# Kernel tuning notes

Measured on AMD Instinct MI355X. Metric: run time of the kernel, lower is better.

The kernel has to match this reference:

```python
import jax, jax.numpy as jnp
import numpy as np

LN_EPS = 1e-5

def _next_fast_len(n):
    # smallest 5-smooth integer >= n (matches scipy.fftpack.next_fast_len)
    while True:
        m = n
        for p in (2, 3, 5):
            while m % p == 0:
                m //= p
        if m == 1:
            return n
        n += 1

def _conv1d_fft(x, w):
    # x: (b, h, N, d), convolved along axis -2 against w: (h, M) along axis -1.
    # Matches the torch reference: multiply by conj(rfft(w)), roll by -1, take last N.
    N = x.shape[-2]
    M = w.shape[-1]
    L = _next_fast_len(N + M - 1)
    fx = jnp.fft.rfft(x, n=L, axis=-2)                    # (b, h, F, d) complex
    fw = jnp.fft.rfft(w, n=L, axis=-1)                    # (h, F) complex
    out = jnp.fft.irfft(fx * jnp.conj(fw)[..., None], L, axis=-2)
    out = jnp.roll(out, -1, axis=-2)
    return out[..., L - N:, :]                            # (b, h, N, d)

def setup_inputs() -> dict:
    key = jax.random.key(0)
    ks = jax.random.split(key, 5)
    b, n, d, h = 4, 4096, 1024, 8
    dh = d // h
    s = 0.02
    return {
        "x": jax.random.normal(ks[0], (b, n, d), jnp.float32),
        "ln_gamma": jnp.ones((d,), jnp.float32),
        "ln_beta": jnp.zeros((d,), jnp.float32),
        "w_in": jax.random.normal(ks[1], (d, d), jnp.float32) * s,
        "b_in": jnp.zeros((d,), jnp.float32),
        "initial_state": jax.random.normal(ks[2], (h, dh), jnp.float32),
        "alpha": jax.random.normal(ks[3], (h,), jnp.float32),
        "w_out": jax.random.normal(ks[4], (d, d), jnp.float32) * s,
        "b_out": jnp.zeros((d,), jnp.float32),
    }

def reference(x, ln_gamma, ln_beta, w_in, b_in, initial_state, alpha, w_out, b_out):
    b, n, d = x.shape
    h, dh = initial_state.shape
    # LayerNorm
    mu = jnp.mean(x, axis=-1, keepdims=True)
    var = jnp.mean((x - mu) ** 2, axis=-1, keepdims=True)
    xn = (x - mu) * jax.lax.rsqrt(var + LN_EPS) * ln_gamma + ln_beta
    # project_in (torch Linear: y = x @ W.T + b)
    xp = xn @ w_in.T + b_in
    # b n (h d) -> b h n d
    xh = xp.reshape(b, n, h, dh).transpose(0, 2, 1, 3)
    # prepend learned initial state, then first difference along n
    init = jnp.broadcast_to(initial_state[None, :, None, :], (b, h, 1, dh))
    xc = jnp.concatenate([init, xh], axis=2)
    xd = xc[:, :, 1:] - xc[:, :, :-1]                     # (b, h, n, dh)
    # EMA weights per head
    a = jax.nn.sigmoid(alpha)[:, None]                    # (h, 1)
    ar = jnp.arange(n)
    w = a * (1.0 - a) ** ar[::-1]                         # (h, n)
    out = _conv1d_fft(xd, w)
    # initial-state contribution
    init_w = (1.0 - a) ** (ar + 1)                        # (h, n)
    out = out + init_w[:, :, None] * initial_state[:, None, :]
    # b h n d -> b n (h d), then project_out
    out = out.transpose(0, 2, 1, 3).reshape(b, n, d)
    return out @ w_out.T + b_out
```

## Files before the change

kernel.cpp:

```cpp
#include <hip/hip_runtime.h>
#include <stdint.h>

typedef float  f32x4 __attribute__((ext_vector_type(4)));
typedef __bf16 bf16x8 __attribute__((ext_vector_type(8)));
typedef short  s16x8 __attribute__((ext_vector_type(8)));
typedef unsigned short u16;

static __device__ __forceinline__ u16 f2bf(float f) {
  unsigned u = __float_as_uint(f);
  u += 0x7fffu + ((u >> 16) & 1u);
  return (u16)(u >> 16);
}
static __device__ __forceinline__ float bf2f(u16 u) {
  return __uint_as_float(((unsigned)u) << 16);
}

static __device__ __forceinline__ void async_copy16(void* lds, const void* g) {
  __builtin_amdgcn_global_load_lds(
      (const __attribute__((address_space(1))) unsigned int*)g,
      (__attribute__((address_space(3))) unsigned int*)lds, 16, 0, 0);
}

__global__ __launch_bounds__(256) void cvt2_k(const float* __restrict__ in0,
                                              const float* __restrict__ in1,
                                              u16* __restrict__ out0,
                                              u16* __restrict__ out1, int n4) {
  int i = blockIdx.x * 256 + threadIdx.x;
  const float* in = (i < n4) ? in0 : in1;
  u16* out = (i < n4) ? out0 : out1;
  int idx = (i < n4) ? i : i - n4;
  float4 v = reinterpret_cast<const float4*>(in)[idx];
  ushort4 o;
  o.x = f2bf(v.x); o.y = f2bf(v.y); o.z = f2bf(v.z); o.w = f2bf(v.w);
  reinterpret_cast<ushort4*>(out)[idx] = o;
}

__global__ __launch_bounds__(256) void ln_k(const float* __restrict__ x,
                                            const float* __restrict__ g,
                                            const float* __restrict__ b,
                                            u16* __restrict__ xn) {
  const int D = 1024;
  const int row = blockIdx.x;
  const int tid = threadIdx.x;
  const float4 v = reinterpret_cast<const float4*>(x + (size_t)row * D)[tid];
  float s  = v.x + v.y + v.z + v.w;
  float s2 = v.x * v.x + v.y * v.y + v.z * v.z + v.w * v.w;
  #pragma unroll
  for (int off = 32; off > 0; off >>= 1) {
    s  += __shfl_down(s, off);
    s2 += __shfl_down(s2, off);
  }
  __shared__ float red[8];
  const int lane = tid & 63, wv = tid >> 6;
  if (lane == 0) { red[wv] = s; red[4 + wv] = s2; }
  __syncthreads();
  s  = red[0] + red[1] + red[2] + red[3];
  s2 = red[4] + red[5] + red[6] + red[7];
  const float mu   = s * (1.0f / D);
  const float var  = s2 * (1.0f / D) - mu * mu;
  const float rstd = rsqrtf(var + 1e-5f);
  const float4 gv = reinterpret_cast<const float4*>(g)[tid];
  const float4 bv = reinterpret_cast<const float4*>(b)[tid];
  ushort4 o;
  o.x = f2bf((v.x - mu) * rstd * gv.x + bv.x);
  o.y = f2bf((v.y - mu) * rstd * gv.y + bv.y);
  o.z = f2bf((v.z - mu) * rstd * gv.z + bv.z);
  o.w = f2bf((v.w - mu) * rstd * gv.w + bv.w);
  reinterpret_cast<ushort4*>(xn + (size_t)row * D)[tid] = o;
}

template<int MODE>
__global__ __launch_bounds__(512, 2) void gemm_bt_k(const u16* __restrict__ A,
                                                    const u16* __restrict__ Bm,
                                                    const float* __restrict__ bias,
                                                    void* __restrict__ Cv,
                                                    const float* __restrict__ alpha,
                                                    float* __restrict__ Lp,
                                                    int M, int N, int K) {
  const int tid  = threadIdx.x;
  const int lane = tid & 63;
  const int wv   = tid >> 6;
  const int wrr  = wv >> 2;
  const int wcc  = wv & 3;
  const int ntN  = N >> 8;
  const int nwg  = (M >> 8) * ntN;
  const int bid  = blockIdx.x;
  const int wgid = (bid & 7) * (nwg >> 3) + (bid >> 3);
  const int mt = wgid / ntN, nt = wgid % ntN;
  const int m0 = mt << 8, n0 = nt << 8;

  __shared__ __align__(16) u16 smem[65536];
  __shared__ float sRed[256];

  const int u   = tid >> 3;
  const int tch = tid & 7;
  const int csw = (tch ^ (u & 7)) << 3;
  const int lofs = u * 64 + (tch << 3);
  const u16* gA = A  + (size_t)(m0 + u) * K + csw;
  const u16* gB = Bm + (size_t)(n0 + u) * K + csw;

  f32x4 acc[8][4];
  #pragma unroll
  for (int i = 0; i < 8; ++i)
    #pragma unroll
    for (int j = 0; j < 4; ++j) acc[i][j] = f32x4{0.f, 0.f, 0.f, 0.f};

  const int fr  = lane & 15;
  const int fkc = lane >> 4;
  const int sx  = fr & 7;
  const int nk  = K >> 6;
  int buf = 0;

  #pragma unroll
  for (int r = 0; r < 4; ++r) {
    async_copy16(&smem[lofs + r * 4096], gA + (size_t)(r * 64) * K);
    async_copy16(&smem[32768 + lofs + r * 4096], gB + (size_t)(r * 64) * K);
  }
  __syncthreads();

  for (int t = 0; t < nk; ++t) {
    if (t + 1 < nk) {
      const size_t ko = (size_t)(t + 1) << 6;
      const int nb = (buf ^ 1) * 16384;
      #pragma unroll
      for (int r = 0; r < 4; ++r) {
        async_copy16(&smem[nb + lofs + r * 4096], gA + ko + (size_t)(r * 64) * K);
        async_copy16(&smem[32768 + nb + lofs + r * 4096], gB + ko + (size_t)(r * 64) * K);
      }
    }
    const u16* bA = smem + buf * 16384;
    const u16* bB = smem + 32768 + buf * 16384;
    #pragma unroll
    for (int s = 0; s < 2; ++s) {
      const int ch = ((((s << 2) + fkc) ^ sx) << 3);
      s16x8 af[8], bfr[4];
      #pragma unroll
      for (int i = 0; i < 8; ++i)
        af[i] = *reinterpret_cast<const s16x8*>(
            &bA[(wrr * 128 + i * 16 + fr) * 64 + ch]);
      #pragma unroll
      for (int j = 0; j < 4; ++j)
        bfr[j] = *reinterpret_cast<const s16x8*>(
            &bB[(wcc * 64 + j * 16 + fr) * 64 + ch]);
      #pragma unroll
      for (int i = 0; i < 8; ++i)
        #pragma unroll
        for (int j = 0; j < 4; ++j)
          acc[i][j] = __builtin_amdgcn_mfma_f32_16x16x32_bf16(
              __builtin_bit_cast(bf16x8, af[i]),
              __builtin_bit_cast(bf16x8, bfr[j]), acc[i][j], 0, 0, 0);
    }
    __syncthreads();
    buf ^= 1;
  }

  float* sC = (float*)smem;
  const int cr = (lane >> 4) << 2;
  const int cc = lane & 15;
  float bv[4];
  #pragma unroll
  for (int nj = 0; nj < 4; ++nj) bv[nj] = bias[n0 + wcc * 64 + nj * 16 + cc];

  #pragma unroll
  for (int p = 0; p < 2; ++p) {
    __syncthreads();
    if (wrr == p) {
      #pragma unroll
      for (int mi = 0; mi < 8; ++mi)
        #pragma unroll
        for (int nj = 0; nj < 4; ++nj)
          #pragma unroll
          for (int rr = 0; rr < 4; ++rr) {
            const int row = mi * 16 + cr + rr;
            const int col = wcc * 64 + nj * 16 + cc;
            sC[row * 256 + (col ^ ((row & 4) << 2))] = acc[mi][nj][rr] + bv[nj];
          }
    }
    __syncthreads();
    #pragma unroll 4
    for (int it = 0; it < 16; ++it) {
      const int row  = it * 8 + (tid >> 6);
      const int col0 = (tid & 63) * 4;
      f32x4 v = *(const f32x4*)&sC[row * 256 + (col0 ^ ((row & 4) << 2))];
      const size_t goff = (size_t)(m0 + p * 128 + row) * N + n0 + col0;
      if (MODE == 1) {
        ushort4 o; o.x = f2bf(v[0]); o.y = f2bf(v[1]); o.z = f2bf(v[2]); o.w = f2bf(v[3]);
        *(ushort4*)&((u16*)Cv)[goff] = o;
      } else {
        *(f32x4*)&((float*)Cv)[goff] = v;
      }
    }
    if (MODE == 1) {
      const int col = tid & 255;
      const int hh = (n0 + col) >> 7;
      const float a  = 1.0f / (1.0f + __expf(-alpha[hh]));
      const float rw = 1.0f - a;
      float r64 = rw;
      #pragma unroll
      for (int s = 0; s < 6; ++s) r64 *= r64;
      const bool lo = (tid < 256);
      const int rbase  = lo ? 1 : 64;
      const int nsteps = lo ? 63 : 64;
      float prev = sC[(rbase - 1) * 256 + (col ^ (((rbase - 1) & 4) << 2))];
      float L = 0.f;
      #pragma unroll 8
      for (int t = rbase; t < rbase + 64; ++t) {
        if (t - rbase >= nsteps) break;
        const float w = sC[t * 256 + (col ^ ((t & 4) << 2))];
        L = rw * L + a * (w - prev);
        prev = w;
      }
      if (!lo) sRed[col] = L;
      __syncthreads();
      if (lo) {
        const float Lt = r64 * L + sRed[col];
        const int bb = m0 >> 12;
        const int q  = ((m0 >> 7) & 31) + p;
        Lp[((size_t)bb * 32 + q) * 1024 + n0 + col] = Lt;
      }
    }
  }
}

__global__ __launch_bounds__(256) void ema_carry_k(const u16* __restrict__ xpb,
                                                   const float* __restrict__ alpha,
                                                   const float* __restrict__ init,
                                                   float* __restrict__ carry) {
  const int Dd = 1024, nCh = 32;
  const int idx = blockIdx.x * 256 + threadIdx.x;
  const int c  = idx & (Dd - 1);
  const int bb = idx >> 10;
  const int h = c >> 7;
  const float a = 1.0f / (1.0f + __expf(-alpha[h]));
  const float r = 1.0f - a;
  float q_ = r, r127 = 1.0f;
  #pragma unroll
  for (int s = 0; s < 7; ++s) { r127 *= q_; q_ *= q_; }
  const float rT = r127 * r;
  float cin = init[c];
  float prevv = cin;
  for (int q = 0; q < nCh; ++q) {
    const size_t rowb = (size_t)bb * 4096 + (size_t)q * 128;
    const float v0 = bf2f(xpb[rowb * Dd + c]);
    const size_t off = ((size_t)bb * nCh + q) * Dd + c;
    const float L = carry[off] + a * r127 * (v0 - prevv);
    carry[off] = cin;
    cin = rT * cin + L;
    prevv = bf2f(xpb[(rowb + 127) * Dd + c]);
  }
}

__global__ __launch_bounds__(256) void ema_apply_k(const u16* __restrict__ xp,
                                                   const float* __restrict__ alpha,
                                                   const float* __restrict__ init,
                                                   const float* __restrict__ carry,
                                                   u16* __restrict__ ob) {
  const int Nn = 4096, Dd = 1024, T = 128, nCh = 32;
  int bid = blockIdx.x;
  const int cg = bid & 1;  bid >>= 1;
  const int q  = bid & 31; bid >>= 5;
  const int bb = bid;
  const int c = cg * 512 + threadIdx.x * 2;
  const int h = c >> 7;
  const float a = 1.0f / (1.0f + __expf(-alpha[h]));
  const float r = 1.0f - a;
  const u16* px = xp + ((size_t)bb * Nn + (size_t)q * T) * Dd + c;
  u16* po = ob + ((size_t)bb * Nn + (size_t)q * T) * Dd + c;
  float2 Oin = *(const float2*)(carry + ((size_t)bb * nCh + q) * Dd + c);
  float O0 = Oin.x, O1 = Oin.y;
  float p0, p1;
  if (q == 0) { p0 = init[c]; p1 = init[c + 1]; }
  else { ushort2 pv = *(const ushort2*)(px - Dd); p0 = bf2f(pv.x); p1 = bf2f(pv.y); }
  #pragma unroll 4
  for (int t = 0; t < T; ++t) {
    ushort2 v = *(const ushort2*)(px + (size_t)t * Dd);
    float v0 = bf2f(v.x), v1 = bf2f(v.y);
    O0 = r * O0 + a * (v0 - p0);
    O1 = r * O1 + a * (v1 - p1);
    p0 = v0; p1 = v1;
    ushort2 o; o.x = f2bf(O0); o.y = f2bf(O1);
    *(ushort2*)(po + (size_t)t * Dd) = o;
  }
}

extern "C" void kernel_launch(void* const* d_in, const int* in_sizes, int n_in,
                              void* d_out, int out_size, void* d_ws, size_t ws_size,
                              hipStream_t stream) {
  const float* x     = (const float*)d_in[0];
  const float* ln_g  = (const float*)d_in[1];
  const float* ln_b  = (const float*)d_in[2];
  const float* w_in  = (const float*)d_in[3];
  const float* b_in  = (const float*)d_in[4];
  const float* init  = (const float*)d_in[5];
  const float* alpha = (const float*)d_in[6];
  const float* w_out = (const float*)d_in[7];
  const float* b_out = (const float*)d_in[8];
  float* out = (float*)d_out;

  const int B = 4, N = 4096, D = 1024;
  const int M = B * N;

  char* p = (char*)d_ws;
  u16*   xn  = (u16*)p; p += (size_t)M * D * sizeof(u16);
  u16*   wi  = (u16*)p; p += (size_t)D * D * sizeof(u16);
  u16*   wo  = (u16*)p; p += (size_t)D * D * sizeof(u16);
  u16*   xpb = (u16*)p; p += (size_t)M * D * sizeof(u16);
  float* cr  = (float*)p; p += (size_t)B * 32 * D * sizeof(float);
  u16*   ob  = (u16*)p;

  const int n4 = D * D / 4;
  cvt2_k<<<dim3(2 * n4 / 256), dim3(256), 0, stream>>>(w_in, w_out, wi, wo, n4);
  ln_k<<<dim3(M), dim3(256), 0, stream>>>(x, ln_g, ln_b, xn);
  gemm_bt_k<1><<<dim3((M / 256) * (D / 256)), dim3(512), 0, stream>>>(
      xn, wi, b_in, xpb, alpha, cr, M, D, D);
  ema_carry_k<<<dim3(B * D / 256), dim3(256), 0, stream>>>(xpb, alpha, init, cr);
  ema_apply_k<<<dim3(B * 32 * 2), dim3(256), 0, stream>>>(xpb, alpha, init, cr, ob);
  gemm_bt_k<0><<<dim3((M / 256) * (D / 256)), dim3(512), 0, stream>>>(
      ob, wo, b_out, out, nullptr, nullptr, M, D, D);
}
```

Measured before the change: 138.8 us.

## Fuse weight conversion into LayerNorm, prefetch carry loads, widen EMA apply grid

Three changes. First, the weight bf16 conversion kernel is merged into the LayerNorm kernel as extra blocks, which saves one launch. Second, ema_carry_k now loads all 32 chunk values into registers before running the serial recurrence, so the global loads are not stalled behind the dependency chain. Third, ema_apply_k now gives each thread one channel instead of two and launches twice as many blocks, for more parallelism at the cost of narrower 2-byte memory accesses.

```diff
diff --git a/kernel.cpp b/kernel.cpp
--- a/kernel.cpp
+++ b/kernel.cpp
@@ -21,27 +21,28 @@
       (__attribute__((address_space(3))) unsigned int*)lds, 16, 0, 0);
 }
 
-__global__ __launch_bounds__(256) void cvt2_k(const float* __restrict__ in0,
-                                              const float* __restrict__ in1,
-                                              u16* __restrict__ out0,
-                                              u16* __restrict__ out1, int n4) {
-  int i = blockIdx.x * 256 + threadIdx.x;
-  const float* in = (i < n4) ? in0 : in1;
-  u16* out = (i < n4) ? out0 : out1;
-  int idx = (i < n4) ? i : i - n4;
-  float4 v = reinterpret_cast<const float4*>(in)[idx];
-  ushort4 o;
-  o.x = f2bf(v.x); o.y = f2bf(v.y); o.z = f2bf(v.z); o.w = f2bf(v.w);
-  reinterpret_cast<ushort4*>(out)[idx] = o;
-}
-
-__global__ __launch_bounds__(256) void ln_k(const float* __restrict__ x,
-                                            const float* __restrict__ g,
-                                            const float* __restrict__ b,
-                                            u16* __restrict__ xn) {
-  const int D = 1024;
+__global__ __launch_bounds__(256) void ln_cvt_k(const float* __restrict__ x,
+                                                const float* __restrict__ g,
+                                                const float* __restrict__ b,
+                                                u16* __restrict__ xn,
+                                                const float* __restrict__ w0,
+                                                const float* __restrict__ w1,
+                                                u16* __restrict__ o0,
+                                                u16* __restrict__ o1) {
+  const int D = 1024, Mrows = 16384, n4 = 262144;
+  const int tid = threadIdx.x;
+  if (blockIdx.x >= Mrows) {
+    int i = (blockIdx.x - Mrows) * 256 + tid;
+    const float* in = (i < n4) ? w0 : w1;
+    u16* out = (i < n4) ? o0 : o1;
+    int idx = (i < n4) ? i : i - n4;
+    float4 v = reinterpret_cast<const float4*>(in)[idx];
+    ushort4 o;
+    o.x = f2bf(v.x); o.y = f2bf(v.y); o.z = f2bf(v.z); o.w = f2bf(v.w);
+    reinterpret_cast<ushort4*>(out)[idx] = o;
+    return;
+  }
   const int row = blockIdx.x;
-  const int tid = threadIdx.x;
   const float4 v = reinterpret_cast<const float4*>(x + (size_t)row * D)[tid];
   float s  = v.x + v.y + v.z + v.w;
   float s2 = v.x * v.x + v.y * v.y + v.z * v.z + v.w * v.w;
@@ -237,16 +238,22 @@
   #pragma unroll
   for (int s = 0; s < 7; ++s) { r127 *= q_; q_ *= q_; }
   const float rT = r127 * r;
+  float L[32], v0[32], vm[32];
+  #pragma unroll
+  for (int q = 0; q < nCh; ++q) {
+    const size_t rowb = (size_t)bb * 4096 + (size_t)q * 128;
+    L[q]  = carry[((size_t)bb * nCh + q) * Dd + c];
+    v0[q] = bf2f(xpb[rowb * Dd + c]);
+    vm[q] = bf2f(xpb[(rowb + 127) * Dd + c]);
+  }
   float cin = init[c];
   float prevv = cin;
+  #pragma unroll
   for (int q = 0; q < nCh; ++q) {
-    const size_t rowb = (size_t)bb * 4096 + (size_t)q * 128;
-    const float v0 = bf2f(xpb[rowb * Dd + c]);
-    const size_t off = ((size_t)bb * nCh + q) * Dd + c;
-    const float L = carry[off] + a * r127 * (v0 - prevv);
-    carry[off] = cin;
-    cin = rT * cin + L;
-    prevv = bf2f(xpb[(rowb + 127) * Dd + c]);
+    const float Lf = L[q] + a * r127 * (v0[q] - prevv);
+    carry[((size_t)bb * nCh + q) * Dd + c] = cin;
+    cin = rT * cin + Lf;
+    prevv = vm[q];
   }
 }
 
@@ -257,29 +264,23 @@
                                                    u16* __restrict__ ob) {
   const int Nn = 4096, Dd = 1024, T = 128, nCh = 32;
   int bid = blockIdx.x;
-  const int cg = bid & 1;  bid >>= 1;
+  const int cg = bid & 3;  bid >>= 2;
   const int q  = bid & 31; bid >>= 5;
   const int bb = bid;
-  const int c = cg * 512 + threadIdx.x * 2;
+  const int c = cg * 256 + threadIdx.x;
   const int h = c >> 7;
   const float a = 1.0f / (1.0f + __expf(-alpha[h]));
   const float r = 1.0f - a;
   const u16* px = xp + ((size_t)bb * Nn + (size_t)q * T) * Dd + c;
   u16* po = ob + ((size_t)bb * Nn + (size_t)q * T) * Dd + c;
-  float2 Oin = *(const float2*)(carry + ((size_t)bb * nCh + q) * Dd + c);
-  float O0 = Oin.x, O1 = Oin.y;
-  float p0, p1;
-  if (q == 0) { p0 = init[c]; p1 = init[c + 1]; }
-  else { ushort2 pv = *(const ushort2*)(px - Dd); p0 = bf2f(pv.x); p1 = bf2f(pv.y); }
+  float O = carry[((size_t)bb * nCh + q) * Dd + c];
+  float p0 = (q == 0) ? init[c] : bf2f(px[-Dd]);
   #pragma unroll 4
   for (int t = 0; t < T; ++t) {
-    ushort2 v = *(const ushort2*)(px + (size_t)t * Dd);
-    float v0 = bf2f(v.x), v1 = bf2f(v.y);
-    O0 = r * O0 + a * (v0 - p0);
-    O1 = r * O1 + a * (v1 - p1);
-    p0 = v0; p1 = v1;
-    ushort2 o; o.x = f2bf(O0); o.y = f2bf(O1);
-    *(ushort2*)(po + (size_t)t * Dd) = o;
+    const float v = bf2f(px[(size_t)t * Dd]);
+    O = r * O + a * (v - p0);
+    p0 = v;
+    po[(size_t)t * Dd] = f2bf(O);
   }
 }
 
@@ -308,13 +309,12 @@
   float* cr  = (float*)p; p += (size_t)B * 32 * D * sizeof(float);
   u16*   ob  = (u16*)p;
 
-  const int n4 = D * D / 4;
-  cvt2_k<<<dim3(2 * n4 / 256), dim3(256), 0, stream>>>(w_in, w_out, wi, wo, n4);
-  ln_k<<<dim3(M), dim3(256), 0, stream>>>(x, ln_g, ln_b, xn);
+  ln_cvt_k<<<dim3(M + 2048), dim3(256), 0, stream>>>(
+      x, ln_g, ln_b, xn, w_in, w_out, wi, wo);
   gemm_bt_k<1><<<dim3((M / 256) * (D / 256)), dim3(512), 0, stream>>>(
       xn, wi, b_in, xpb, alpha, cr, M, D, D);
   ema_carry_k<<<dim3(B * D / 256), dim3(256), 0, stream>>>(xpb, alpha, init, cr);
-  ema_apply_k<<<dim3(B * 32 * 2), dim3(256), 0, stream>>>(xpb, alpha, init, cr, ob);
+  ema_apply_k<<<dim3(B * 32 * 4), dim3(256), 0, stream>>>(xpb, alpha, init, cr, ob);
   gemm_bt_k<0><<<dim3((M / 256) * (D / 256)), dim3(512), 0, stream>>>(
       ob, wo, b_out, out, nullptr, nullptr, M, D, D);
 }
```

New measurement: 137.5 us, median of 2. No clear change (-0.9%).
